# Kernel tuning notes

Measured on AMD Instinct MI355X. Metric: run time of the kernel, lower is better.

Reference implementation:

```python
import jax, jax.numpy as jnp
import numpy as np

S, N, D = 8, 2048, 256

def setup_inputs() -> dict:
    key = jax.random.key(0)
    k0, k1, k2 = jax.random.split(key, 3)
    tensor0 = jax.random.normal(k0, (S, N, D), dtype=jnp.float32)
    tensor1 = jax.random.normal(k1, (S, N, D), dtype=jnp.float32)
    # glorot-ish scale for the (D, D) bilinear kernel
    kernel = jax.random.normal(k2, (D, D), dtype=jnp.float32) * (1.0 / np.sqrt(D))
    bias = jnp.zeros((1,), dtype=jnp.float32)  # scalar bias, shape () in keras
    return {"tensor0": tensor0, "tensor1": tensor1, "kernel": kernel, "bias": bias}

def reference(tensor0, tensor1, kernel, bias):
    # Faithful math of Bilinear(bilin_axes=[1]) on inputs [S, N, D]:
    # out[s, i, j] = sum_{d,e} tensor1[s,i,d] * kernel[d,e] * tensor0[s,j,e] + bias
    # (the original builds the full [S,N,S,N] cross tensor and extracts the
    #  batch diagonal; this einsum is the equivalent O(S*N*N*D) contraction).
    qt0 = jnp.einsum('de,sje->sjd', kernel, tensor0)      # [S, N, D]
    out = jnp.einsum('sid,sjd->sij', tensor1, qt0)        # [S, N, N]
    return out + bias[0]
```

## Files before the change

kernel.cpp:

```cpp
#include <hip/hip_runtime.h>
#include <hip/hip_bf16.h>


typedef __bf16 bf16x8 __attribute__((ext_vector_type(8)));
typedef float f32x4 __attribute__((ext_vector_type(4)));

__device__ __forceinline__ unsigned short f2bf(float f) {
  union { __hip_bfloat16 h; unsigned short u; } v;
  v.h = __float2bfloat16(f);
  return v.u;
}

__global__ __launch_bounds__(256) void cvt3(const float4* __restrict__ t0,
                                            const float4* __restrict__ t1,
                                            const float4* __restrict__ kk,
                                            ushort4* __restrict__ o0,
                                            ushort4* __restrict__ o1,
                                            ushort4* __restrict__ ok) {
  const int stride = gridDim.x * blockDim.x;
  const int i0 = blockIdx.x * blockDim.x + threadIdx.x;
  for (int j = i0; j < 1048576; j += stride) {
    float4 v = t0[j];
    o0[j] = make_ushort4(f2bf(v.x), f2bf(v.y), f2bf(v.z), f2bf(v.w));
  }
  for (int j = i0; j < 1048576; j += stride) {
    float4 v = t1[j];
    o1[j] = make_ushort4(f2bf(v.x), f2bf(v.y), f2bf(v.z), f2bf(v.w));
  }
  for (int j = i0; j < 16384; j += stride) {
    float4 v = kk[j];
    ok[j] = make_ushort4(f2bf(v.x), f2bf(v.y), f2bf(v.z), f2bf(v.w));
  }
}

template <bool OUT_BF16>
__global__ __launch_bounds__(256, 2) void gemm_nt(
    const unsigned short* __restrict__ A, const unsigned short* __restrict__ B,
    void* __restrict__ Cout, const float* __restrict__ bias,
    const int K, const int ldc,
    const long long aStride, const long long bStride, const long long cStride) {
  __shared__ unsigned short sA[2][128 * 32];
  __shared__ unsigned short sB[2][128 * 32];

  const int tid = threadIdx.x;
  const int wave = tid >> 6;
  const int lane = tid & 63;
  const int quad = lane >> 4;
  const int l16 = lane & 15;
  const int wrow = (wave >> 1) * 64;
  const int wcol = (wave & 1) * 64;

  const int brow = blockIdx.y * 128;
  const int bcol = blockIdx.x * 128;
  const long long bz = blockIdx.z;

  const unsigned short* Ab = A + bz * aStride + (long long)brow * K;
  const unsigned short* Bb = B + bz * bStride + (long long)bcol * K;

  const int srow = wave * 16 + (lane >> 2);
  const int scol = (lane & 3) * 8;

  auto stage = [&](unsigned short* dA, unsigned short* dB, int kt) {
#pragma unroll
    for (int half = 0; half < 2; half++) {
      const unsigned short* ga = Ab + (long long)(half * 64 + srow) * K + kt + scol;
      const unsigned short* gb = Bb + (long long)(half * 64 + srow) * K + kt + scol;
      __builtin_amdgcn_global_load_lds(
          (const __attribute__((address_space(1))) unsigned int*)ga,
          (__attribute__((address_space(3))) unsigned int*)(dA + (half * 64 + wave * 16) * 32),
          16, 0, 0);
      __builtin_amdgcn_global_load_lds(
          (const __attribute__((address_space(1))) unsigned int*)gb,
          (__attribute__((address_space(3))) unsigned int*)(dB + (half * 64 + wave * 16) * 32),
          16, 0, 0);
    }
  };

  f32x4 acc[4][4];
#pragma unroll
  for (int i = 0; i < 4; i++)
#pragma unroll
    for (int j = 0; j < 4; j++) acc[i][j] = (f32x4){0.f, 0.f, 0.f, 0.f};

  stage(sA[0], sB[0], 0);

  for (int kt = 0; kt < K; kt += 64) {
    __syncthreads();
    {
      bf16x8 af[4], bfr[4];
#pragma unroll
      for (int mi = 0; mi < 4; mi++)
        af[mi] = *(const bf16x8*)&sA[0][(wrow + mi * 16 + l16) * 32 + quad * 8];
#pragma unroll
      for (int ni = 0; ni < 4; ni++)
        bfr[ni] = *(const bf16x8*)&sB[0][(wcol + ni * 16 + l16) * 32 + quad * 8];
      stage(sA[1], sB[1], kt + 32);
#pragma unroll
      for (int mi = 0; mi < 4; mi++)
#pragma unroll
        for (int ni = 0; ni < 4; ni++)
          acc[mi][ni] = __builtin_amdgcn_mfma_f32_16x16x32_bf16(
              af[mi], bfr[ni], acc[mi][ni], 0, 0, 0);
    }
    __syncthreads();
    {
      bf16x8 af[4], bfr[4];
#pragma unroll
      for (int mi = 0; mi < 4; mi++)
        af[mi] = *(const bf16x8*)&sA[1][(wrow + mi * 16 + l16) * 32 + quad * 8];
#pragma unroll
      for (int ni = 0; ni < 4; ni++)
        bfr[ni] = *(const bf16x8*)&sB[1][(wcol + ni * 16 + l16) * 32 + quad * 8];
      if (kt + 64 < K) stage(sA[0], sB[0], kt + 64);
#pragma unroll
      for (int mi = 0; mi < 4; mi++)
#pragma unroll
        for (int ni = 0; ni < 4; ni++)
          acc[mi][ni] = __builtin_amdgcn_mfma_f32_16x16x32_bf16(
              af[mi], bfr[ni], acc[mi][ni], 0, 0, 0);
    }
  }

  if constexpr (OUT_BF16) {
    unsigned short* C = (unsigned short*)Cout + bz * cStride;
#pragma unroll
    for (int mi = 0; mi < 4; mi++)
#pragma unroll
      for (int ni = 0; ni < 4; ni++) {
        const int r0 = brow + wrow + mi * 16 + quad * 4;
        const int c = bcol + wcol + ni * 16 + l16;
#pragma unroll
        for (int r = 0; r < 4; r++)
          C[(long long)(r0 + r) * ldc + c] = f2bf(acc[mi][ni][r]);
      }
  } else {
    const float bv = bias[0];
    float* C = (float*)Cout + bz * cStride;
#pragma unroll
    for (int mi = 0; mi < 4; mi++)
#pragma unroll
      for (int ni = 0; ni < 4; ni++) {
        const int r0 = brow + wrow + mi * 16 + quad * 4;
        const int c = bcol + wcol + ni * 16 + l16;
#pragma unroll
        for (int r = 0; r < 4; r++)
          C[(long long)(r0 + r) * ldc + c] = acc[mi][ni][r] + bv;
      }
  }
}

extern "C" void kernel_launch(void* const* d_in, const int* in_sizes, int n_in,
                              void* d_out, int out_size, void* d_ws, size_t ws_size,
                              hipStream_t stream) {
  const float* t0 = (const float*)d_in[0];
  const float* t1 = (const float*)d_in[1];
  const float* kk = (const float*)d_in[2];
  const float* bias = (const float*)d_in[3];

  unsigned short* T0b = (unsigned short*)d_ws;
  unsigned short* T1b = T0b + 4194304;
  unsigned short* Kb = T1b + 4194304;
  unsigned short* Qb = Kb + 65536;

  cvt3<<<4096, 256, 0, stream>>>((const float4*)t0, (const float4*)t1,
                                 (const float4*)kk, (ushort4*)T0b,
                                 (ushort4*)T1b, (ushort4*)Kb);

  gemm_nt<true><<<dim3(2, 128, 1), 256, 0, stream>>>(T0b, Kb, Qb, nullptr, 256,
                                                     256, 0, 0, 0);

  gemm_nt<false><<<dim3(16, 16, 8), 256, 0, stream>>>(
      T1b, Qb, d_out, bias, 256, 2048, 524288LL, 524288LL, 4194304LL);
}
```

Baseline: 186.0 us.

## Stage 64-wide K tiles with XOR-swizzled LDS layout in bilinear GEMM

The LDS tile grows from 32 to 64 K-elements per row and stays double-buffered, so each barrier now covers 64 K elements instead of 32, halving the number of __syncthreads per K iteration. Global-to-LDS loads place each 16-byte chunk at a column XOR-swizzled by row, and fragment reads apply the matching XOR so ds_read accesses spread across banks. LDS use doubles to 64 KB per block, which could limit the two blocks per CU that the launch bounds request.

```diff
diff --git a/kernel.cpp b/kernel.cpp
--- a/kernel.cpp
+++ b/kernel.cpp
@@ -39,8 +39,8 @@
     void* __restrict__ Cout, const float* __restrict__ bias,
     const int K, const int ldc,
     const long long aStride, const long long bStride, const long long cStride) {
-  __shared__ unsigned short sA[2][128 * 32];
-  __shared__ unsigned short sB[2][128 * 32];
+  __shared__ unsigned short sA[2][128 * 64];
+  __shared__ unsigned short sB[2][128 * 64];
 
   const int tid = threadIdx.x;
   const int wave = tid >> 6;
@@ -49,6 +49,7 @@
   const int l16 = lane & 15;
   const int wrow = (wave >> 1) * 64;
   const int wcol = (wave & 1) * 64;
+  const int rsw = (l16 & 7) * 8;
 
   const int brow = blockIdx.y * 128;
   const int bcol = blockIdx.x * 128;
@@ -57,21 +58,22 @@
   const unsigned short* Ab = A + bz * aStride + (long long)brow * K;
   const unsigned short* Bb = B + bz * bStride + (long long)bcol * K;
 
-  const int srow = wave * 16 + (lane >> 2);
-  const int scol = (lane & 3) * 8;
+  const int srow = lane >> 3;
+  const int scol = ((lane & 7) ^ srow) * 8;
 
   auto stage = [&](unsigned short* dA, unsigned short* dB, int kt) {
 #pragma unroll
-    for (int half = 0; half < 2; half++) {
-      const unsigned short* ga = Ab + (long long)(half * 64 + srow) * K + kt + scol;
-      const unsigned short* gb = Bb + (long long)(half * 64 + srow) * K + kt + scol;
+    for (int i = 0; i < 4; i++) {
+      const int r = i * 32 + wave * 8;
+      const unsigned short* ga = Ab + (long long)(r + srow) * K + kt + scol;
+      const unsigned short* gb = Bb + (long long)(r + srow) * K + kt + scol;
       __builtin_amdgcn_global_load_lds(
           (const __attribute__((address_space(1))) unsigned int*)ga,
-          (__attribute__((address_space(3))) unsigned int*)(dA + (half * 64 + wave * 16) * 32),
+          (__attribute__((address_space(3))) unsigned int*)(dA + r * 64),
           16, 0, 0);
       __builtin_amdgcn_global_load_lds(
           (const __attribute__((address_space(1))) unsigned int*)gb,
-          (__attribute__((address_space(3))) unsigned int*)(dB + (half * 64 + wave * 16) * 32),
+          (__attribute__((address_space(3))) unsigned int*)(dB + r * 64),
           16, 0, 0);
     }
   };
@@ -84,17 +86,24 @@
 
   stage(sA[0], sB[0], 0);
 
+  int cur = 0;
   for (int kt = 0; kt < K; kt += 64) {
     __syncthreads();
+    const unsigned short* a = sA[cur];
+    const unsigned short* b = sB[cur];
     {
       bf16x8 af[4], bfr[4];
 #pragma unroll
-      for (int mi = 0; mi < 4; mi++)
-        af[mi] = *(const bf16x8*)&sA[0][(wrow + mi * 16 + l16) * 32 + quad * 8];
+      for (int mi = 0; mi < 4; mi++) {
+        const int row = wrow + mi * 16 + l16;
+        af[mi] = *(const bf16x8*)&a[row * 64 + ((quad * 8) ^ rsw)];
+      }
 #pragma unroll
-      for (int ni = 0; ni < 4; ni++)
-        bfr[ni] = *(const bf16x8*)&sB[0][(wcol + ni * 16 + l16) * 32 + quad * 8];
-      stage(sA[1], sB[1], kt + 32);
+      for (int ni = 0; ni < 4; ni++) {
+        const int row = wcol + ni * 16 + l16;
+        bfr[ni] = *(const bf16x8*)&b[row * 64 + ((quad * 8) ^ rsw)];
+      }
+      if (kt + 64 < K) stage(sA[cur ^ 1], sB[cur ^ 1], kt + 64);
 #pragma unroll
       for (int mi = 0; mi < 4; mi++)
 #pragma unroll
@@ -102,16 +111,18 @@
           acc[mi][ni] = __builtin_amdgcn_mfma_f32_16x16x32_bf16(
               af[mi], bfr[ni], acc[mi][ni], 0, 0, 0);
     }
-    __syncthreads();
     {
       bf16x8 af[4], bfr[4];
 #pragma unroll
-      for (int mi = 0; mi < 4; mi++)
-        af[mi] = *(const bf16x8*)&sA[1][(wrow + mi * 16 + l16) * 32 + quad * 8];
+      for (int mi = 0; mi < 4; mi++) {
+        const int row = wrow + mi * 16 + l16;
+        af[mi] = *(const bf16x8*)&a[row * 64 + ((32 + quad * 8) ^ rsw)];
+      }
 #pragma unroll
-      for (int ni = 0; ni < 4; ni++)
-        bfr[ni] = *(const bf16x8*)&sB[1][(wcol + ni * 16 + l16) * 32 + quad * 8];
-      if (kt + 64 < K) stage(sA[0], sB[0], kt + 64);
+      for (int ni = 0; ni < 4; ni++) {
+        const int row = wcol + ni * 16 + l16;
+        bfr[ni] = *(const bf16x8*)&b[row * 64 + ((32 + quad * 8) ^ rsw)];
+      }
 #pragma unroll
       for (int mi = 0; mi < 4; mi++)
 #pragma unroll
@@ -119,6 +130,7 @@
           acc[mi][ni] = __builtin_amdgcn_mfma_f32_16x16x32_bf16(
               af[mi], bfr[ni], acc[mi][ni], 0, 0, 0);
     }
+    cur ^= 1;
   }
 
   if constexpr (OUT_BF16) {
```

Result: no change. 184.9 us (-0.5%).
